# Performance work log

Measured on AMD Instinct MI355X. Metric: run time of the kernel, lower is better.

## Reference

```python
import jax, jax.numpy as jnp
import numpy as np

B, C, H, W = 32, 1024, 32, 32  # N = H*W must equal C for the attn_c * attn_s broadcast
C8 = C // 8


def setup_inputs() -> dict:
    key = jax.random.key(0)
    ks = jax.random.split(key, 9)
    s = 1.0 / np.sqrt(C)
    return {
        "z": jax.random.normal(ks[0], (B, C, H, W), jnp.float32),
        "x": jax.random.normal(ks[1], (B, C, H, W), jnp.float32),
        "y": jax.random.normal(ks[2], (B, C, H, W), jnp.float32),
        "Wq": jax.random.normal(ks[3], (C8, C), jnp.float32) * s,
        "bq": jax.random.normal(ks[4], (C8,), jnp.float32) * 0.01,
        "Wk": jax.random.normal(ks[5], (C8, C), jnp.float32) * s,
        "bk": jax.random.normal(ks[6], (C8,), jnp.float32) * 0.01,
        "Wv": jax.random.normal(ks[7], (C, C), jnp.float32) * s,
        "bv": jax.random.normal(ks[8], (C,), jnp.float32) * 0.01,
    }


def reference(z, x, y, Wq, bq, Wk, bk, Wv, bv):
    b, c, h, w = x.shape
    n = h * w
    xf = x.reshape(b, c, n)
    yf = y.reshape(b, c, n)
    zf = z.reshape(b, c, n)

    # 1x1 convs == channel matmuls
    q = jnp.einsum('oc,bcn->bon', Wq, xf) + bq[None, :, None]   # (B, C/8, N)
    k = jnp.einsum('oc,bcn->bon', Wk, yf) + bk[None, :, None]   # (B, C/8, N)

    # channel-projected spatial attention: (B, N, N)
    energy_c = jnp.einsum('bcn,bcm->bnm', q, k)
    attention_c = jax.nn.softmax(energy_c, axis=-1)

    # raw channel attention: (B, C, C)
    energy_s = jnp.einsum('bcn,bdn->bcd', xf, yf)
    energy_s = jnp.max(energy_s, axis=-1, keepdims=True) - energy_s
    attention_s = jax.nn.softmax(energy_s, axis=-1)

    # multiplicative combine + third softmax (requires N == C)
    attention = jax.nn.softmax(attention_c * attention_s, axis=-1)

    v = jnp.einsum('oc,bcn->bon', Wv, zf) + bv[None, :, None]   # (B, C, N)
    # out[b,c,m] = sum_n v[b,c,n] * attention[b,m,n]  (value @ attention^T)
    out = jnp.einsum('bcn,bmn->bcm', v, attention)
    return z + out.reshape(b, c, h, w)
```

## Files before the change

### kernel.cpp

```cpp
#include <hip/hip_runtime.h>
#include <hip/hip_bf16.h>

typedef __attribute__((ext_vector_type(8))) short s8_t;
typedef __attribute__((ext_vector_type(4))) float f4_t;

__device__ __forceinline__ unsigned short f2bf(float f) {
  union { float f; unsigned u; } x; x.f = f;
  unsigned r = x.u + 0x7fffu + ((x.u >> 16) & 1u);
  return (unsigned short)(r >> 16);
}

__device__ __forceinline__ void split2(float e0, float e1, unsigned& hp, unsigned& lp) {
  unsigned b0 = __float_as_uint(e0), b1 = __float_as_uint(e1);
  unsigned h0 = b0 & 0xFFFF0000u, h1 = b1 & 0xFFFF0000u;
  hp = (b0 >> 16) | h1;
  float l0 = e0 - __uint_as_float(h0), l1 = e1 - __uint_as_float(h1);
  lp = (__float_as_uint(l0) >> 16) | (__float_as_uint(l1) & 0xFFFF0000u);
}

__device__ __forceinline__ void gload16(const void* g, void* l) {
  __builtin_amdgcn_global_load_lds(
      (const __attribute__((address_space(1))) void*)g,
      (__attribute__((address_space(3))) void*)l, 16, 0, 0);
}

__global__ __launch_bounds__(256) void k_convert(const float* __restrict__ in,
                                                 unsigned short* __restrict__ out, int n) {
  int i = (blockIdx.x * 256 + threadIdx.x) * 8;
  if (i >= n) return;
  float4 a = *(const float4*)(in + i);
  float4 b = *(const float4*)(in + i + 4);
  ushort4 u0; u0.x = f2bf(a.x); u0.y = f2bf(a.y); u0.z = f2bf(a.z); u0.w = f2bf(a.w);
  ushort4 u1; u1.x = f2bf(b.x); u1.y = f2bf(b.y); u1.z = f2bf(b.z); u1.w = f2bf(b.w);
  *(ushort4*)(out + i) = u0;
  *(ushort4*)(out + i + 4) = u1;
}

__global__ __launch_bounds__(256) void k_transp32(const float* __restrict__ in,
                                                  float* __restrict__ out) {
  __shared__ float tile[64][65];
  const int t = threadIdx.x, b = blockIdx.z;
  const int r0 = blockIdx.y * 64, c0 = blockIdx.x * 64;
  const float* ip = in + (size_t)b * 1048576;
  float* op = out + (size_t)b * 1048576;
  const int tr = t >> 4, tc = (t & 15) * 4;
#pragma unroll
  for (int p = 0; p < 4; ++p) {
    int r = p * 16 + tr;
    float4 v = *(const float4*)(ip + (size_t)(r0 + r) * 1024 + c0 + tc);
    tile[r][tc] = v.x; tile[r][tc + 1] = v.y; tile[r][tc + 2] = v.z; tile[r][tc + 3] = v.w;
  }
  __syncthreads();
#pragma unroll
  for (int p = 0; p < 4; ++p) {
    int n = p * 16 + tr;
    float4 w;
    w.x = tile[tc][n]; w.y = tile[tc + 1][n]; w.z = tile[tc + 2][n]; w.w = tile[tc + 3][n];
    *(float4*)(op + (size_t)(c0 + n) * 1024 + r0 + tc) = w;
  }
}

__global__ __launch_bounds__(256) void k_transpbf(const float* __restrict__ in,
                                                  unsigned short* __restrict__ outt) {
  __shared__ unsigned short tile[64][72];
  const int t = threadIdx.x, b = blockIdx.z;
  const int r0 = blockIdx.y * 64, c0 = blockIdx.x * 64;
  const float* ip = in + (size_t)b * 1048576;
  const int tr = t >> 4, tc = (t & 15) * 4;
#pragma unroll
  for (int p = 0; p < 4; ++p) {
    int r = p * 16 + tr;
    float4 v = *(const float4*)(ip + (size_t)(r0 + r) * 1024 + c0 + tc);
    tile[r][tc] = f2bf(v.x); tile[r][tc + 1] = f2bf(v.y);
    tile[r][tc + 2] = f2bf(v.z); tile[r][tc + 3] = f2bf(v.w);
  }
  __syncthreads();
#pragma unroll
  for (int p = 0; p < 4; ++p) {
    int n = p * 16 + tr;
    ushort4 w;
    w.x = tile[tc][n]; w.y = tile[tc + 1][n]; w.z = tile[tc + 2][n]; w.w = tile[tc + 3][n];
    *(ushort4*)(outt + (size_t)b * 1048576 + (size_t)(c0 + n) * 1024 + r0 + tc) = w;
  }
}

template <int BIAS_MODE>
__global__ __launch_bounds__(256) void k_mfma3(
    const float* __restrict__ A, int lda, long long sA,
    const float* __restrict__ B, int ldb, long long sB,
    float* __restrict__ C, int ldc, long long sC,
    const float* __restrict__ bias, int K) {
  __shared__ __align__(16) unsigned short Ah[4096], Al[4096], Bh[4096], Bl[4096];
  const int tid = threadIdx.x;
  const int lane = tid & 63, wave = tid >> 6;
  const int wr = wave >> 1, wc = wave & 1;
  const int bz = blockIdx.z;
  const int m0 = blockIdx.x * 128, n0 = blockIdx.y * 128;

  const int sr = tid >> 1, sh = (tid & 1) * 16;
  const float* ag = A + (long long)bz * sA + (long long)(m0 + sr) * lda + sh;
  const float* bg = B + (long long)bz * sB + (long long)(n0 + sr) * ldb + sh;
  unsigned short* wah = &Ah[sr * 32 + sh];
  unsigned short* wal = &Al[sr * 32 + sh];
  unsigned short* wbh = &Bh[sr * 32 + sh];
  unsigned short* wbl = &Bl[sr * 32 + sh];

  const int lr = lane & 15, lg = lane >> 4;
  const int fa = (wr * 64 + lr) * 32 + lg * 8;
  const int fb = (wc * 64 + lr) * 32 + lg * 8;

  f4_t acc[4][4];
#pragma unroll
  for (int i = 0; i < 4; ++i)
#pragma unroll
    for (int j = 0; j < 4; ++j) acc[i][j] = (f4_t)0.f;

  for (int k0 = 0; k0 < K; k0 += 32) {
    float av[16], bv[16];
#pragma unroll
    for (int p = 0; p < 4; ++p) {
      *(float4*)(av + p * 4) = *(const float4*)(ag + p * 4);
      *(float4*)(bv + p * 4) = *(const float4*)(bg + p * 4);
    }
    unsigned ah[8], al[8], bh[8], bl[8];
#pragma unroll
    for (int p = 0; p < 8; ++p) {
      split2(av[2 * p], av[2 * p + 1], ah[p], al[p]);
      split2(bv[2 * p], bv[2 * p + 1], bh[p], bl[p]);
    }
    *(uint4*)(wah) = *(uint4*)(ah);     *(uint4*)(wah + 8) = *(uint4*)(ah + 4);
    *(uint4*)(wal) = *(uint4*)(al);     *(uint4*)(wal + 8) = *(uint4*)(al + 4);
    *(uint4*)(wbh) = *(uint4*)(bh);     *(uint4*)(wbh + 8) = *(uint4*)(bh + 4);
    *(uint4*)(wbl) = *(uint4*)(bl);     *(uint4*)(wbl + 8) = *(uint4*)(bl + 4);
    ag += 32; bg += 32;
    __syncthreads();

    s8_t fah[4], fbh[4], ftmp[4];
#pragma unroll
    for (int f = 0; f < 4; ++f) {
      fah[f] = *(const s8_t*)(Ah + fa + f * 512);
      fbh[f] = *(const s8_t*)(Bh + fb + f * 512);
    }
#pragma unroll
    for (int i = 0; i < 4; ++i)
#pragma unroll
      for (int j = 0; j < 4; ++j)
        acc[i][j] = __builtin_amdgcn_mfma_f32_16x16x32_bf16(fah[i], fbh[j], acc[i][j], 0, 0, 0);
#pragma unroll
    for (int f = 0; f < 4; ++f) ftmp[f] = *(const s8_t*)(Bl + fb + f * 512);
#pragma unroll
    for (int i = 0; i < 4; ++i)
#pragma unroll
      for (int j = 0; j < 4; ++j)
        acc[i][j] = __builtin_amdgcn_mfma_f32_16x16x32_bf16(fah[i], ftmp[j], acc[i][j], 0, 0, 0);
#pragma unroll
    for (int f = 0; f < 4; ++f) ftmp[f] = *(const s8_t*)(Al + fa + f * 512);
#pragma unroll
    for (int i = 0; i < 4; ++i)
#pragma unroll
      for (int j = 0; j < 4; ++j)
        acc[i][j] = __builtin_amdgcn_mfma_f32_16x16x32_bf16(ftmp[i], fbh[j], acc[i][j], 0, 0, 0);
    __syncthreads();
  }

#pragma unroll
  for (int i = 0; i < 4; ++i) {
    const int rbase = m0 + wr * 64 + i * 16 + lg * 4;
#pragma unroll
    for (int j = 0; j < 4; ++j) {
      const int col = n0 + wc * 64 + j * 16 + lr;
      float bc = (BIAS_MODE == 2) ? bias[col] : 0.f;
#pragma unroll
      for (int e = 0; e < 4; ++e) {
        float v = acc[i][j][e];
        if (BIAS_MODE == 2) v += bc;
        C[(long long)bz * sC + (long long)(rbase + e) * ldc + col] = v;
      }
    }
  }
}

template <int BIAS_MODE, bool OUT_BF16, bool RESID>
__global__ __launch_bounds__(256) void k_mfma(
    const unsigned short* __restrict__ A, int lda, long long sA,
    const unsigned short* __restrict__ B, int ldb, long long sB,
    void* __restrict__ Cp, int ldc, long long sC,
    const float* __restrict__ bias,
    const float* __restrict__ resid, long long sR, int K) {
  __shared__ __align__(16) unsigned short As[4096];
  __shared__ __align__(16) unsigned short Bs[4096];
  const int tid = threadIdx.x;
  const int lane = tid & 63, wave = tid >> 6;
  const int wr = wave >> 1, wc = wave & 1;
  const int bz = blockIdx.z;
  const int m0 = blockIdx.x * 128, n0 = blockIdx.y * 128;

  const int ch0 = wave * 64 + lane, ch1 = ch0 + 256;
  const unsigned short* pa0 = A + (long long)bz * sA + (long long)(m0 + (ch0 >> 2)) * lda + (ch0 & 3) * 8;
  const unsigned short* pa1 = A + (long long)bz * sA + (long long)(m0 + (ch1 >> 2)) * lda + (ch1 & 3) * 8;
  const unsigned short* pb0 = B + (long long)bz * sB + (long long)(n0 + (ch0 >> 2)) * ldb + (ch0 & 3) * 8;
  const unsigned short* pb1 = B + (long long)bz * sB + (long long)(n0 + (ch1 >> 2)) * ldb + (ch1 & 3) * 8;
  char* la0 = (char*)As + wave * 1024;
  char* la1 = la0 + 4096;
  char* lb0 = (char*)Bs + wave * 1024;
  char* lb1 = lb0 + 4096;

  const int lr = lane & 15, lg = lane >> 4;
  const unsigned short* arp = As + (wr * 64 + lr) * 32 + lg * 8;
  const unsigned short* brp = Bs + (wc * 64 + lr) * 32 + lg * 8;

  f4_t acc[4][4];
#pragma unroll
  for (int i = 0; i < 4; ++i)
#pragma unroll
    for (int j = 0; j < 4; ++j) acc[i][j] = (f4_t)0.f;

  for (int k0 = 0; k0 < K; k0 += 32) {
    gload16(pa0, la0); gload16(pa1, la1);
    gload16(pb0, lb0); gload16(pb1, lb1);
    pa0 += 32; pa1 += 32; pb0 += 32; pb1 += 32;
    __syncthreads();
    s8_t af[4], bf[4];
#pragma unroll
    for (int f = 0; f < 4; ++f) {
      af[f] = *(const s8_t*)(arp + f * 16 * 32);
      bf[f] = *(const s8_t*)(brp + f * 16 * 32);
    }
#pragma unroll
    for (int i = 0; i < 4; ++i)
#pragma unroll
      for (int j = 0; j < 4; ++j)
        acc[i][j] = __builtin_amdgcn_mfma_f32_16x16x32_bf16(af[i], bf[j], acc[i][j], 0, 0, 0);
    __syncthreads();
  }

#pragma unroll
  for (int i = 0; i < 4; ++i) {
    const int rbase = m0 + wr * 64 + i * 16 + lg * 4;
#pragma unroll
    for (int j = 0; j < 4; ++j) {
      const int col = n0 + wc * 64 + j * 16 + lr;
#pragma unroll
      for (int e = 0; e < 4; ++e) {
        const int row = rbase + e;
        float v = acc[i][j][e];
        if (BIAS_MODE == 1) v += bias[row];
        const long long off = (long long)bz * sC + (long long)row * ldc + col;
        if (RESID) v += resid[(long long)bz * sR + (long long)row * ldc + col];
        if (OUT_BF16) ((unsigned short*)Cp)[off] = f2bf(v);
        else          ((float*)Cp)[off] = v;
      }
    }
  }
}

__device__ __forceinline__ float wave_red_max(float v) {
#pragma unroll
  for (int o = 32; o > 0; o >>= 1) v = fmaxf(v, __shfl_down(v, o, 64));
  return v;
}
__device__ __forceinline__ float wave_red_sum(float v) {
#pragma unroll
  for (int o = 32; o > 0; o >>= 1) v += __shfl_down(v, o, 64);
  return v;
}
__device__ __forceinline__ float block_red_max(float v, float* red) {
  v = wave_red_max(v);
  if ((threadIdx.x & 63) == 0) red[threadIdx.x >> 6] = v;
  __syncthreads();
  v = fmaxf(fmaxf(red[0], red[1]), fmaxf(red[2], red[3]));
  __syncthreads();
  return v;
}
__device__ __forceinline__ float block_red_sum(float v, float* red) {
  v = wave_red_sum(v);
  if ((threadIdx.x & 63) == 0) red[threadIdx.x >> 6] = v;
  __syncthreads();
  v = red[0] + red[1] + red[2] + red[3];
  __syncthreads();
  return v;
}

__global__ __launch_bounds__(256) void k_combine(float* __restrict__ ec,
                                                 const float* __restrict__ es) {
  __shared__ float red[4];
  const size_t row = blockIdx.x;
  float* cp = ec + row * 1024;
  const float* sp = es + row * 1024;
  const int tid = threadIdx.x;
  float4 c4 = ((const float4*)cp)[tid];
  float4 s4 = ((const float4*)sp)[tid];

  float mx = fmaxf(fmaxf(c4.x, c4.y), fmaxf(c4.z, c4.w));
  mx = block_red_max(mx, red);
  float e0 = __expf(c4.x - mx), e1 = __expf(c4.y - mx);
  float e2 = __expf(c4.z - mx), e3 = __expf(c4.w - mx);
  float sc = block_red_sum(e0 + e1 + e2 + e3, red);

  float t0 = -s4.x, t1 = -s4.y, t2 = -s4.z, t3 = -s4.w;
  float mt = fmaxf(fmaxf(t0, t1), fmaxf(t2, t3));
  mt = block_red_max(mt, red);
  float f0 = __expf(t0 - mt), f1 = __expf(t1 - mt);
  float f2 = __expf(t2 - mt), f3 = __expf(t3 - mt);
  float ss = block_red_sum(f0 + f1 + f2 + f3, red);

  const float rc = 1.f / sc, rs = 1.f / ss;
  float g0 = __expf((e0 * rc) * (f0 * rs));
  float g1 = __expf((e1 * rc) * (f1 * rs));
  float g2 = __expf((e2 * rc) * (f2 * rs));
  float g3 = __expf((e3 * rc) * (f3 * rs));
  float s3 = block_red_sum(g0 + g1 + g2 + g3, red);
  const float r3 = 1.f / s3;
  ushort4 o;
  o.x = f2bf(g0 * r3); o.y = f2bf(g1 * r3); o.z = f2bf(g2 * r3); o.w = f2bf(g3 * r3);
  ((ushort4*)cp)[tid] = o;
}

extern "C" void kernel_launch(void* const* d_in, const int* in_sizes, int n_in,
                              void* d_out, int out_size, void* d_ws, size_t ws_size,
                              hipStream_t stream) {
  const float* z = (const float*)d_in[0];
  const float* x = (const float*)d_in[1];
  const float* y = (const float*)d_in[2];
  const float* Wq = (const float*)d_in[3];
  const float* bq = (const float*)d_in[4];
  const float* Wk = (const float*)d_in[5];
  const float* bk = (const float*)d_in[6];
  const float* Wv = (const float*)d_in[7];
  const float* bv = (const float*)d_in[8];
  float* out = (float*)d_out;

  char* ws = (char*)d_ws;
  float* es = (float*)ws;
  unsigned short* z_t = (unsigned short*)ws;
  unsigned short* v_bf = z_t + 33554432;
  char* wsB = ws + 134217728;
  float* xytf = (float*)wsB;
  float* ec = (float*)wsB;
  unsigned short* attn = (unsigned short*)wsB;
  char* wsC = ws + 268435456;
  float* q_t = (float*)wsC;
  float* k_t = q_t + 4194304;
  unsigned short* wv = (unsigned short*)wsC;

  dim3 blk(256);
  hipLaunchKernelGGL(k_transp32, dim3(16, 16, 32), blk, 0, stream, x, xytf);
  hipLaunchKernelGGL((k_mfma3<2>), dim3(8, 1, 32), blk, 0, stream,
                     xytf, 1024, 1048576LL, Wq, 1024, 0LL, q_t, 128, 131072LL, bq, 1024);
  hipLaunchKernelGGL(k_transp32, dim3(16, 16, 32), blk, 0, stream, y, xytf);
  hipLaunchKernelGGL((k_mfma3<2>), dim3(8, 1, 32), blk, 0, stream,
                     xytf, 1024, 1048576LL, Wk, 1024, 0LL, k_t, 128, 131072LL, bk, 1024);
  hipLaunchKernelGGL((k_mfma3<0>), dim3(8, 8, 32), blk, 0, stream,
                     x, 1024, 1048576LL, y, 1024, 1048576LL, es, 1024, 1048576LL,
                     (const float*)nullptr, 1024);
  hipLaunchKernelGGL((k_mfma3<0>), dim3(8, 8, 32), blk, 0, stream,
                     q_t, 128, 131072LL, k_t, 128, 131072LL, ec, 1024, 1048576LL,
                     (const float*)nullptr, 128);
  hipLaunchKernelGGL(k_combine, dim3(32768), blk, 0, stream, ec, es);
  hipLaunchKernelGGL(k_transpbf, dim3(16, 16, 32), blk, 0, stream, z, z_t);
  hipLaunchKernelGGL(k_convert, dim3(512), blk, 0, stream, Wv, wv, 1048576);
  hipLaunchKernelGGL((k_mfma<1, true, false>), dim3(8, 8, 32), blk, 0, stream,
                     wv, 1024, 0LL, z_t, 1024, 1048576LL, (void*)v_bf, 1024, 1048576LL,
                     bv, (const float*)nullptr, 0LL, 1024);
  hipLaunchKernelGGL((k_mfma<0, false, true>), dim3(8, 8, 32), blk, 0, stream,
                     v_bf, 1024, 1048576LL, attn, 2048, 2097152LL, (void*)out, 1024, 1048576LL,
                     (const float*)nullptr, z, 1048576LL, 1024);
}
```

Before: 885.7 us.

## Double-buffer LDS tiles in split-bf16 MFMA GEMM to overlap global loads

Converts the 3-pass split-bf16 MFMA GEMM main loop into a software pipeline with two LDS buffers. The next K-tile's global loads are issued before the current tile's MFMAs, and the hi/lo split plus LDS write happen after them. This hides global memory latency and removes one barrier per iteration. In exchange, LDS per block doubles to 64KB, which may reduce occupancy, and register pressure rises from holding the prefetched values.

```diff
diff --git a/kernel.cpp b/kernel.cpp
--- a/kernel.cpp
+++ b/kernel.cpp
@@ -84,13 +84,31 @@
   }
 }
 
+__device__ __forceinline__ void split_write(unsigned short* buf, int wbase,
+                                            const float* av, const float* bv) {
+  unsigned ah[8], al[8], bh[8], bl[8];
+#pragma unroll
+  for (int p = 0; p < 8; ++p) {
+    split2(av[2 * p], av[2 * p + 1], ah[p], al[p]);
+    split2(bv[2 * p], bv[2 * p + 1], bh[p], bl[p]);
+  }
+  *(uint4*)(buf + wbase) = *(uint4*)(ah);
+  *(uint4*)(buf + wbase + 8) = *(uint4*)(ah + 4);
+  *(uint4*)(buf + 4096 + wbase) = *(uint4*)(al);
+  *(uint4*)(buf + 4096 + wbase + 8) = *(uint4*)(al + 4);
+  *(uint4*)(buf + 8192 + wbase) = *(uint4*)(bh);
+  *(uint4*)(buf + 8192 + wbase + 8) = *(uint4*)(bh + 4);
+  *(uint4*)(buf + 12288 + wbase) = *(uint4*)(bl);
+  *(uint4*)(buf + 12288 + wbase + 8) = *(uint4*)(bl + 4);
+}
+
 template <int BIAS_MODE>
 __global__ __launch_bounds__(256) void k_mfma3(
     const float* __restrict__ A, int lda, long long sA,
     const float* __restrict__ B, int ldb, long long sB,
     float* __restrict__ C, int ldc, long long sC,
     const float* __restrict__ bias, int K) {
-  __shared__ __align__(16) unsigned short Ah[4096], Al[4096], Bh[4096], Bl[4096];
+  __shared__ __align__(16) unsigned short sm[32768];
   const int tid = threadIdx.x;
   const int lane = tid & 63, wave = tid >> 6;
   const int wr = wave >> 1, wc = wave & 1;
@@ -100,10 +118,7 @@
   const int sr = tid >> 1, sh = (tid & 1) * 16;
   const float* ag = A + (long long)bz * sA + (long long)(m0 + sr) * lda + sh;
   const float* bg = B + (long long)bz * sB + (long long)(n0 + sr) * ldb + sh;
-  unsigned short* wah = &Ah[sr * 32 + sh];
-  unsigned short* wal = &Al[sr * 32 + sh];
-  unsigned short* wbh = &Bh[sr * 32 + sh];
-  unsigned short* wbl = &Bl[sr * 32 + sh];
+  const int wbase = sr * 32 + sh;
 
   const int lr = lane & 15, lg = lane >> 4;
   const int fa = (wr * 64 + lr) * 32 + lg * 8;
@@ -115,31 +130,39 @@
 #pragma unroll
     for (int j = 0; j < 4; ++j) acc[i][j] = (f4_t)0.f;
 
-  for (int k0 = 0; k0 < K; k0 += 32) {
-    float av[16], bv[16];
-#pragma unroll
-    for (int p = 0; p < 4; ++p) {
-      *(float4*)(av + p * 4) = *(const float4*)(ag + p * 4);
-      *(float4*)(bv + p * 4) = *(const float4*)(bg + p * 4);
-    }
-    unsigned ah[8], al[8], bh[8], bl[8];
-#pragma unroll
-    for (int p = 0; p < 8; ++p) {
-      split2(av[2 * p], av[2 * p + 1], ah[p], al[p]);
-      split2(bv[2 * p], bv[2 * p + 1], bh[p], bl[p]);
-    }
-    *(uint4*)(wah) = *(uint4*)(ah);     *(uint4*)(wah + 8) = *(uint4*)(ah + 4);
-    *(uint4*)(wal) = *(uint4*)(al);     *(uint4*)(wal + 8) = *(uint4*)(al + 4);
-    *(uint4*)(wbh) = *(uint4*)(bh);     *(uint4*)(wbh + 8) = *(uint4*)(bh + 4);
-    *(uint4*)(wbl) = *(uint4*)(bl);     *(uint4*)(wbl + 8) = *(uint4*)(bl + 4);
-    ag += 32; bg += 32;
-    __syncthreads();
-
+  const int nt = K >> 5;
+  float av[16], bv[16];
+
+#pragma unroll
+  for (int p = 0; p < 4; ++p) {
+    *(float4*)(av + p * 4) = *(const float4*)(ag + p * 4);
+    *(float4*)(bv + p * 4) = *(const float4*)(bg + p * 4);
+  }
+  ag += 32; bg += 32;
+  split_write(sm, wbase, av, bv);
+  __syncthreads();
+
+  for (int t = 0; t < nt; ++t) {
+    unsigned short* bufc = sm + (t & 1) * 16384;
+    unsigned short* bufn = sm + ((t + 1) & 1) * 16384;
+    const bool more = (t + 1 < nt);
+    if (more) {
+#pragma unroll
+      for (int p = 0; p < 4; ++p) {
+        *(float4*)(av + p * 4) = *(const float4*)(ag + p * 4);
+        *(float4*)(bv + p * 4) = *(const float4*)(bg + p * 4);
+      }
+      ag += 32; bg += 32;
+    }
+    const unsigned short* Ahp = bufc;
+    const unsigned short* Alp = bufc + 4096;
+    const unsigned short* Bhp = bufc + 8192;
+    const unsigned short* Blp = bufc + 12288;
     s8_t fah[4], fbh[4], ftmp[4];
 #pragma unroll
     for (int f = 0; f < 4; ++f) {
-      fah[f] = *(const s8_t*)(Ah + fa + f * 512);
-      fbh[f] = *(const s8_t*)(Bh + fb + f * 512);
+      fah[f] = *(const s8_t*)(Ahp + fa + f * 512);
+      fbh[f] = *(const s8_t*)(Bhp + fb + f * 512);
     }
 #pragma unroll
     for (int i = 0; i < 4; ++i)
@@ -147,19 +170,20 @@
       for (int j = 0; j < 4; ++j)
         acc[i][j] = __builtin_amdgcn_mfma_f32_16x16x32_bf16(fah[i], fbh[j], acc[i][j], 0, 0, 0);
 #pragma unroll
-    for (int f = 0; f < 4; ++f) ftmp[f] = *(const s8_t*)(Bl + fb + f * 512);
+    for (int f = 0; f < 4; ++f) ftmp[f] = *(const s8_t*)(Blp + fb + f * 512);
 #pragma unroll
     for (int i = 0; i < 4; ++i)
 #pragma unroll
       for (int j = 0; j < 4; ++j)
         acc[i][j] = __builtin_amdgcn_mfma_f32_16x16x32_bf16(fah[i], ftmp[j], acc[i][j], 0, 0, 0);
 #pragma unroll
-    for (int f = 0; f < 4; ++f) ftmp[f] = *(const s8_t*)(Al + fa + f * 512);
+    for (int f = 0; f < 4; ++f) ftmp[f] = *(const s8_t*)(Alp + fa + f * 512);
 #pragma unroll
     for (int i = 0; i < 4; ++i)
 #pragma unroll
       for (int j = 0; j < 4; ++j)
         acc[i][j] = __builtin_amdgcn_mfma_f32_16x16x32_bf16(ftmp[i], fbh[j], acc[i][j], 0, 0, 0);
+    if (more) split_write(bufn, wbase, av, bv);
     __syncthreads();
   }
 
```

Result: slower. 953.9 us (+7.7%).

## Pre-split fp32 inputs to bf16 hi/lo planes and stream via LDS loads

Applied to the files above, without the earlier changes.

Adds a transpose-and-split kernel that writes x and y as bf16 high/low planes in both layouts. The 3-pass bf16 GEMMs then load the planes straight into LDS with global_load_lds instead of converting fp32 in registers each K-step. Q and K projections are fused into one launch that emits split outputs, and batches run in chunks of 8 so the split buffers fit the workspace. A swizzled block-index mapping is added to the GEMMs for better cache locality. In exchange it writes and rereads more intermediate data and issues more small launches.

```diff
diff --git a/kernel.cpp b/kernel.cpp
--- a/kernel.cpp
+++ b/kernel.cpp
@@ -8,6 +8,14 @@
   union { float f; unsigned u; } x; x.f = f;
   unsigned r = x.u + 0x7fffu + ((x.u >> 16) & 1u);
   return (unsigned short)(r >> 16);
+}
+
+__device__ __forceinline__ void split1(float v, unsigned short& h, unsigned short& l) {
+  unsigned b = __float_as_uint(v);
+  unsigned hb = b & 0xFFFF0000u;
+  h = (unsigned short)(b >> 16);
+  float lo = v - __uint_as_float(hb);
+  l = (unsigned short)(__float_as_uint(lo) >> 16);
 }
 
 __device__ __forceinline__ void split2(float e0, float e1, unsigned& hp, unsigned& lp) {
@@ -22,6 +30,17 @@
   __builtin_amdgcn_global_load_lds(
       (const __attribute__((address_space(1))) void*)g,
       (__attribute__((address_space(3))) void*)l, 16, 0, 0);
+}
+
+__device__ __forceinline__ void swz_grid(int& bx, int& by, int& bz) {
+  const int gx = gridDim.x, gy = gridDim.y;
+  const int nwg = gx * gy * gridDim.z;
+  const int flat = (blockIdx.z * gy + blockIdx.y) * gx + blockIdx.x;
+  const int s = (flat & 7) * (nwg >> 3) + (flat >> 3);
+  bx = s % gx;
+  const int r = s / gx;
+  by = r % gy;
+  bz = r / gy;
 }
 
 __global__ __launch_bounds__(256) void k_convert(const float* __restrict__ in,
@@ -36,27 +55,37 @@
   *(ushort4*)(out + i + 4) = u1;
 }
 
-__global__ __launch_bounds__(256) void k_transp32(const float* __restrict__ in,
-                                                  float* __restrict__ out) {
+__global__ __launch_bounds__(256) void k_tsplit(const float* __restrict__ in,
+                                                unsigned short* __restrict__ nh,
+                                                unsigned short* __restrict__ nl,
+                                                unsigned short* __restrict__ th,
+                                                unsigned short* __restrict__ tl) {
   __shared__ float tile[64][65];
-  const int t = threadIdx.x, b = blockIdx.z;
+  const int t = threadIdx.x, bz = blockIdx.z;
   const int r0 = blockIdx.y * 64, c0 = blockIdx.x * 64;
-  const float* ip = in + (size_t)b * 1048576;
-  float* op = out + (size_t)b * 1048576;
+  const float* ip = in + (size_t)bz * 1048576;
+  const size_t ob = (size_t)bz * 1048576;
   const int tr = t >> 4, tc = (t & 15) * 4;
 #pragma unroll
   for (int p = 0; p < 4; ++p) {
     int r = p * 16 + tr;
     float4 v = *(const float4*)(ip + (size_t)(r0 + r) * 1024 + c0 + tc);
+    ushort4 h, l;
+    split1(v.x, h.x, l.x); split1(v.y, h.y, l.y);
+    split1(v.z, h.z, l.z); split1(v.w, h.w, l.w);
+    *(ushort4*)(nh + ob + (size_t)(r0 + r) * 1024 + c0 + tc) = h;
+    *(ushort4*)(nl + ob + (size_t)(r0 + r) * 1024 + c0 + tc) = l;
     tile[r][tc] = v.x; tile[r][tc + 1] = v.y; tile[r][tc + 2] = v.z; tile[r][tc + 3] = v.w;
   }
   __syncthreads();
 #pragma unroll
   for (int p = 0; p < 4; ++p) {
     int n = p * 16 + tr;
-    float4 w;
-    w.x = tile[tc][n]; w.y = tile[tc + 1][n]; w.z = tile[tc + 2][n]; w.w = tile[tc + 3][n];
-    *(float4*)(op + (size_t)(c0 + n) * 1024 + r0 + tc) = w;
+    float a = tile[tc][n], b = tile[tc + 1][n], c = tile[tc + 2][n], d = tile[tc + 3][n];
+    ushort4 h, l;
+    split1(a, h.x, l.x); split1(b, h.y, l.y); split1(c, h.z, l.z); split1(d, h.w, l.w);
+    *(ushort4*)(th + ob + (size_t)(c0 + n) * 1024 + r0 + tc) = h;
+    *(ushort4*)(tl + ob + (size_t)(c0 + n) * 1024 + r0 + tc) = l;
   }
 }
 
@@ -84,26 +113,32 @@
   }
 }
 
-template <int BIAS_MODE>
-__global__ __launch_bounds__(256) void k_mfma3(
-    const float* __restrict__ A, int lda, long long sA,
-    const float* __restrict__ B, int ldb, long long sB,
-    float* __restrict__ C, int ldc, long long sC,
-    const float* __restrict__ bias, int K) {
-  __shared__ __align__(16) unsigned short Ah[4096], Al[4096], Bh[4096], Bl[4096];
-  const int tid = threadIdx.x;
-  const int lane = tid & 63, wave = tid >> 6;
+__global__ __launch_bounds__(256) void k_es3p(
+    const unsigned short* __restrict__ Ah, const unsigned short* __restrict__ Al,
+    long long sA, int lda,
+    const unsigned short* __restrict__ Bh, const unsigned short* __restrict__ Bl,
+    long long sB, int ldb,
+    float* __restrict__ C, int ldc, long long sC, int K) {
+  __shared__ __align__(16) unsigned short smAh[4096], smAl[4096], smBh[4096], smBl[4096];
+  int bx, by, bz; swz_grid(bx, by, bz);
+  const int tid = threadIdx.x, lane = tid & 63, wave = tid >> 6;
   const int wr = wave >> 1, wc = wave & 1;
-  const int bz = blockIdx.z;
-  const int m0 = blockIdx.x * 128, n0 = blockIdx.y * 128;
-
-  const int sr = tid >> 1, sh = (tid & 1) * 16;
-  const float* ag = A + (long long)bz * sA + (long long)(m0 + sr) * lda + sh;
-  const float* bg = B + (long long)bz * sB + (long long)(n0 + sr) * ldb + sh;
-  unsigned short* wah = &Ah[sr * 32 + sh];
-  unsigned short* wal = &Al[sr * 32 + sh];
-  unsigned short* wbh = &Bh[sr * 32 + sh];
-  unsigned short* wbl = &Bl[sr * 32 + sh];
+  const int m0 = bx * 128, n0 = by * 128;
+
+  const int ch0 = wave * 64 + lane, ch1 = ch0 + 256;
+  const int r0 = ch0 >> 2, kc0 = (ch0 & 3) * 8, r1 = ch1 >> 2, kc1 = (ch1 & 3) * 8;
+  const unsigned short* pah0 = Ah + (long long)bz * sA + (long long)(m0 + r0) * lda + kc0;
+  const unsigned short* pah1 = Ah + (long long)bz * sA + (long long)(m0 + r1) * lda + kc1;
+  const unsigned short* pal0 = Al + (long long)bz * sA + (long long)(m0 + r0) * lda + kc0;
+  const unsigned short* pal1 = Al + (long long)bz * sA + (long long)(m0 + r1) * lda + kc1;
+  const unsigned short* pbh0 = Bh + (long long)bz * sB + (long long)(n0 + r0) * ldb + kc0;
+  const unsigned short* pbh1 = Bh + (long long)bz * sB + (long long)(n0 + r1) * ldb + kc1;
+  const unsigned short* pbl0 = Bl + (long long)bz * sB + (long long)(n0 + r0) * ldb + kc0;
+  const unsigned short* pbl1 = Bl + (long long)bz * sB + (long long)(n0 + r1) * ldb + kc1;
+  char* dAh0 = (char*)smAh + wave * 1024; char* dAh1 = dAh0 + 4096;
+  char* dAl0 = (char*)smAl + wave * 1024; char* dAl1 = dAl0 + 4096;
+  char* dBh0 = (char*)smBh + wave * 1024; char* dBh1 = dBh0 + 4096;
+  char* dBl0 = (char*)smBl + wave * 1024; char* dBl1 = dBl0 + 4096;
 
   const int lr = lane & 15, lg = lane >> 4;
   const int fa = (wr * 64 + lr) * 32 + lg * 8;
@@ -116,50 +151,38 @@
     for (int j = 0; j < 4; ++j) acc[i][j] = (f4_t)0.f;
 
   for (int k0 = 0; k0 < K; k0 += 32) {
-    float av[16], bv[16];
-#pragma unroll
-    for (int p = 0; p < 4; ++p) {
-      *(float4*)(av + p * 4) = *(const float4*)(ag + p * 4);
-      *(float4*)(bv + p * 4) = *(const float4*)(bg + p * 4);
+    gload16(pah0, dAh0); gload16(pah1, dAh1);
+    gload16(pal0, dAl0); gload16(pal1, dAl1);
+    gload16(pbh0, dBh0); gload16(pbh1, dBh1);
+    gload16(pbl0, dBl0); gload16(pbl1, dBl1);
+    pah0 += 32; pah1 += 32; pal0 += 32; pal1 += 32;
+    pbh0 += 32; pbh1 += 32; pbl0 += 32; pbl1 += 32;
+    __syncthreads();
+    s8_t fah[4], fbh[4], ft[4];
+#pragma unroll
+    for (int f = 0; f < 4; ++f) {
+      fah[f] = *(const s8_t*)(smAh + fa + f * 512);
+      fbh[f] = *(const s8_t*)(smBh + fb + f * 512);
     }
-    unsigned ah[8], al[8], bh[8], bl[8];
-#pragma unroll
-    for (int p = 0; p < 8; ++p) {
-      split2(av[2 * p], av[2 * p + 1], ah[p], al[p]);
-      split2(bv[2 * p], bv[2 * p + 1], bh[p], bl[p]);
-    }
-    *(uint4*)(wah) = *(uint4*)(ah);     *(uint4*)(wah + 8) = *(uint4*)(ah + 4);
-    *(uint4*)(wal) = *(uint4*)(al);     *(uint4*)(wal + 8) = *(uint4*)(al + 4);
-    *(uint4*)(wbh) = *(uint4*)(bh);     *(uint4*)(wbh + 8) = *(uint4*)(bh + 4);
-    *(uint4*)(wbl) = *(uint4*)(bl);     *(uint4*)(wbl + 8) = *(uint4*)(bl + 4);
-    ag += 32; bg += 32;
-    __syncthreads();
-
-    s8_t fah[4], fbh[4], ftmp[4];
-#pragma unroll
-    for (int f = 0; f < 4; ++f) {
-      fah[f] = *(const s8_t*)(Ah + fa + f * 512);
-      fbh[f] = *(const s8_t*)(Bh + fb + f * 512);
-    }
 #pragma unroll
     for (int i = 0; i < 4; ++i)
 #pragma unroll
       for (int j = 0; j < 4; ++j)
         acc[i][j] = __builtin_amdgcn_mfma_f32_16x16x32_bf16(fah[i], fbh[j], acc[i][j], 0, 0, 0);
 #pragma unroll
-    for (int f = 0; f < 4; ++f) ftmp[f] = *(const s8_t*)(Bl + fb + f * 512);
-#pragma unroll
-    for (int i = 0; i < 4; ++i)
-#pragma unroll
-      for (int j = 0; j < 4; ++j)
-        acc[i][j] = __builtin_amdgcn_mfma_f32_16x16x32_bf16(fah[i], ftmp[j], acc[i][j], 0, 0, 0);
-#pragma unroll
-    for (int f = 0; f < 4; ++f) ftmp[f] = *(const s8_t*)(Al + fa + f * 512);
-#pragma unroll
-    for (int i = 0; i < 4; ++i)
-#pragma unroll
-      for (int j = 0; j < 4; ++j)
-        acc[i][j] = __builtin_amdgcn_mfma_f32_16x16x32_bf16(ftmp[i], fbh[j], acc[i][j], 0, 0, 0);
+    for (int f = 0; f < 4; ++f) ft[f] = *(const s8_t*)(smBl + fb + f * 512);
+#pragma unroll
+    for (int i = 0; i < 4; ++i)
+#pragma unroll
+      for (int j = 0; j < 4; ++j)
+        acc[i][j] = __builtin_amdgcn_mfma_f32_16x16x32_bf16(fah[i], ft[j], acc[i][j], 0, 0, 0);
+#pragma unroll
+    for (int f = 0; f < 4; ++f) ft[f] = *(const s8_t*)(smAl + fa + f * 512);
+#pragma unroll
+    for (int i = 0; i < 4; ++i)
+#pragma unroll
+      for (int j = 0; j < 4; ++j)
+        acc[i][j] = __builtin_amdgcn_mfma_f32_16x16x32_bf16(ft[i], fbh[j], acc[i][j], 0, 0, 0);
     __syncthreads();
   }
 
@@ -169,12 +192,115 @@
 #pragma unroll
     for (int j = 0; j < 4; ++j) {
       const int col = n0 + wc * 64 + j * 16 + lr;
-      float bc = (BIAS_MODE == 2) ? bias[col] : 0.f;
+#pragma unroll
+      for (int e = 0; e < 4; ++e)
+        C[(long long)bz * sC + (long long)(rbase + e) * ldc + col] = acc[i][j][e];
+    }
+  }
+}
+
+__global__ __launch_bounds__(256) void k_qk3p(
+    const unsigned short* __restrict__ Axh, const unsigned short* __restrict__ Axl,
+    const unsigned short* __restrict__ Ayh, const unsigned short* __restrict__ Ayl,
+    const float* __restrict__ Wqf, const float* __restrict__ Wkf,
+    const float* __restrict__ bqf, const float* __restrict__ bkf,
+    unsigned short* __restrict__ Qh, unsigned short* __restrict__ Ql,
+    unsigned short* __restrict__ Kh, unsigned short* __restrict__ Kl) {
+  __shared__ __align__(16) unsigned short smAh[4096], smAl[4096], smBh[4096], smBl[4096];
+  int bx, by, bz; swz_grid(bx, by, bz);
+  const unsigned short* Ah = by ? Ayh : Axh;
+  const unsigned short* Al = by ? Ayl : Axl;
+  const float* Bf = by ? Wkf : Wqf;
+  const float* bias = by ? bkf : bqf;
+  unsigned short* Oh = by ? Kh : Qh;
+  unsigned short* Ol = by ? Kl : Ql;
+
+  const int tid = threadIdx.x, lane = tid & 63, wave = tid >> 6;
+  const int wr = wave >> 1, wc = wave & 1;
+  const int m0 = bx * 128;
+
+  const int ch0 = wave * 64 + lane, ch1 = ch0 + 256;
+  const int r0 = ch0 >> 2, kc0 = (ch0 & 3) * 8, r1 = ch1 >> 2, kc1 = (ch1 & 3) * 8;
+  const unsigned short* pah0 = Ah + (long long)bz * 1048576 + (long long)(m0 + r0) * 1024 + kc0;
+  const unsigned short* pah1 = Ah + (long long)bz * 1048576 + (long long)(m0 + r1) * 1024 + kc1;
+  const unsigned short* pal0 = Al + (long long)bz * 1048576 + (long long)(m0 + r0) * 1024 + kc0;
+  const unsigned short* pal1 = Al + (long long)bz * 1048576 + (long long)(m0 + r1) * 1024 + kc1;
+  char* dAh0 = (char*)smAh + wave * 1024; char* dAh1 = dAh0 + 4096;
+  char* dAl0 = (char*)smAl + wave * 1024; char* dAl1 = dAl0 + 4096;
+
+  const int sr = tid >> 1, sh = (tid & 1) * 16;
+  const float* bg = Bf + (long long)sr * 1024 + sh;
+  const int wbase = sr * 32 + sh;
+
+  const int lr = lane & 15, lg = lane >> 4;
+  const int fa = (wr * 64 + lr) * 32 + lg * 8;
+  const int fb = (wc * 64 + lr) * 32 + lg * 8;
+
+  f4_t acc[4][4];
+#pragma unroll
+  for (int i = 0; i < 4; ++i)
+#pragma unroll
+    for (int j = 0; j < 4; ++j) acc[i][j] = (f4_t)0.f;
+
+  for (int k0 = 0; k0 < 1024; k0 += 32) {
+    gload16(pah0, dAh0); gload16(pah1, dAh1);
+    gload16(pal0, dAl0); gload16(pal1, dAl1);
+    pah0 += 32; pah1 += 32; pal0 += 32; pal1 += 32;
+    float bv[16];
+#pragma unroll
+    for (int p = 0; p < 4; ++p) *(float4*)(bv + p * 4) = *(const float4*)(bg + p * 4);
+    bg += 32;
+    unsigned bh[8], bl[8];
+#pragma unroll
+    for (int p = 0; p < 8; ++p) split2(bv[2 * p], bv[2 * p + 1], bh[p], bl[p]);
+    *(uint4*)(smBh + wbase) = *(uint4*)(bh);
+    *(uint4*)(smBh + wbase + 8) = *(uint4*)(bh + 4);
+    *(uint4*)(smBl + wbase) = *(uint4*)(bl);
+    *(uint4*)(smBl + wbase + 8) = *(uint4*)(bl + 4);
+    __syncthreads();
+    s8_t fah[4], fbh[4], ft[4];
+#pragma unroll
+    for (int f = 0; f < 4; ++f) {
+      fah[f] = *(const s8_t*)(smAh + fa + f * 512);
+      fbh[f] = *(const s8_t*)(smBh + fb + f * 512);
+    }
+#pragma unroll
+    for (int i = 0; i < 4; ++i)
+#pragma unroll
+      for (int j = 0; j < 4; ++j)
+        acc[i][j] = __builtin_amdgcn_mfma_f32_16x16x32_bf16(fah[i], fbh[j], acc[i][j], 0, 0, 0);
+#pragma unroll
+    for (int f = 0; f < 4; ++f) ft[f] = *(const s8_t*)(smBl + fb + f * 512);
+#pragma unroll
+    for (int i = 0; i < 4; ++i)
+#pragma unroll
+      for (int j = 0; j < 4; ++j)
+        acc[i][j] = __builtin_amdgcn_mfma_f32_16x16x32_bf16(fah[i], ft[j], acc[i][j], 0, 0, 0);
+#pragma unroll
+    for (int f = 0; f < 4; ++f) ft[f] = *(const s8_t*)(smAl + fa + f * 512);
+#pragma unroll
+    for (int i = 0; i < 4; ++i)
+#pragma unroll
+      for (int j = 0; j < 4; ++j)
+        acc[i][j] = __builtin_amdgcn_mfma_f32_16x16x32_bf16(ft[i], fbh[j], acc[i][j], 0, 0, 0);
+    __syncthreads();
+  }
+
+#pragma unroll
+  for (int i = 0; i < 4; ++i) {
+    const int rbase = m0 + wr * 64 + i * 16 + lg * 4;
+#pragma unroll
+    for (int j = 0; j < 4; ++j) {
+      const int col = wc * 64 + j * 16 + lr;
+      const float bc = bias[col];
 #pragma unroll
       for (int e = 0; e < 4; ++e) {
-        float v = acc[i][j][e];
-        if (BIAS_MODE == 2) v += bc;
-        C[(long long)bz * sC + (long long)(rbase + e) * ldc + col] = v;
+        float v = acc[i][j][e] + bc;
+        unsigned short h, l;
+        split1(v, h, l);
+        const long long off = (long long)bz * 131072 + (long long)(rbase + e) * 128 + col;
+        Oh[off] = h;
+        Ol[off] = l;
       }
     }
   }
@@ -189,11 +315,11 @@
     const float* __restrict__ resid, long long sR, int K) {
   __shared__ __align__(16) unsigned short As[4096];
   __shared__ __align__(16) unsigned short Bs[4096];
+  int bxs, bys, bz; swz_grid(bxs, bys, bz);
   const int tid = threadIdx.x;
   const int lane = tid & 63, wave = tid >> 6;
   const int wr = wave >> 1, wc = wave & 1;
-  const int bz = blockIdx.z;
-  const int m0 = blockIdx.x * 128, n0 = blockIdx.y * 128;
+  const int m0 = bxs * 128, n0 = bys * 128;
 
   const int ch0 = wave * 64 + lane, ch1 = ch0 + 256;
   const unsigned short* pa0 = A + (long long)bz * sA + (long long)(m0 + (ch0 >> 2)) * lda + (ch0 & 3) * 8;
@@ -335,27 +461,39 @@
   unsigned short* z_t = (unsigned short*)ws;
   unsigned short* v_bf = z_t + 33554432;
   char* wsB = ws + 134217728;
-  float* xytf = (float*)wsB;
+  unsigned short* xh  = (unsigned short*)wsB;
+  unsigned short* xl  = xh + 8388608;
+  unsigned short* yh  = xl + 8388608;
+  unsigned short* yl  = yh + 8388608;
+  unsigned short* xth = yl + 8388608;
+  unsigned short* xtl = xth + 8388608;
+  unsigned short* yth = xtl + 8388608;
+  unsigned short* ytl = yth + 8388608;
   float* ec = (float*)wsB;
   unsigned short* attn = (unsigned short*)wsB;
   char* wsC = ws + 268435456;
-  float* q_t = (float*)wsC;
-  float* k_t = q_t + 4194304;
+  unsigned short* qh = (unsigned short*)wsC;
+  unsigned short* ql = qh + 4194304;
+  unsigned short* kh = ql + 4194304;
+  unsigned short* kl = kh + 4194304;
   unsigned short* wv = (unsigned short*)wsC;
 
   dim3 blk(256);
-  hipLaunchKernelGGL(k_transp32, dim3(16, 16, 32), blk, 0, stream, x, xytf);
-  hipLaunchKernelGGL((k_mfma3<2>), dim3(8, 1, 32), blk, 0, stream,
-                     xytf, 1024, 1048576LL, Wq, 1024, 0LL, q_t, 128, 131072LL, bq, 1024);
-  hipLaunchKernelGGL(k_transp32, dim3(16, 16, 32), blk, 0, stream, y, xytf);
-  hipLaunchKernelGGL((k_mfma3<2>), dim3(8, 1, 32), blk, 0, stream,
-                     xytf, 1024, 1048576LL, Wk, 1024, 0LL, k_t, 128, 131072LL, bk, 1024);
-  hipLaunchKernelGGL((k_mfma3<0>), dim3(8, 8, 32), blk, 0, stream,
-                     x, 1024, 1048576LL, y, 1024, 1048576LL, es, 1024, 1048576LL,
-                     (const float*)nullptr, 1024);
-  hipLaunchKernelGGL((k_mfma3<0>), dim3(8, 8, 32), blk, 0, stream,
-                     q_t, 128, 131072LL, k_t, 128, 131072LL, ec, 1024, 1048576LL,
-                     (const float*)nullptr, 128);
+  for (int c = 0; c < 4; ++c) {
+    const size_t boff = (size_t)c * 8 * 1048576;
+    hipLaunchKernelGGL(k_tsplit, dim3(16, 16, 8), blk, 0, stream, x + boff, xh, xl, xth, xtl);
+    hipLaunchKernelGGL(k_tsplit, dim3(16, 16, 8), blk, 0, stream, y + boff, yh, yl, yth, ytl);
+    hipLaunchKernelGGL(k_es3p, dim3(8, 8, 8), blk, 0, stream,
+                       xh, xl, 1048576LL, 1024, yh, yl, 1048576LL, 1024,
+                       es + boff, 1024, 1048576LL, 1024);
+    hipLaunchKernelGGL(k_qk3p, dim3(8, 2, 8), blk, 0, stream,
+                       xth, xtl, yth, ytl, Wq, Wk, bq, bk,
+                       qh + c * 8 * 131072, ql + c * 8 * 131072,
+                       kh + c * 8 * 131072, kl + c * 8 * 131072);
+  }
+  hipLaunchKernelGGL(k_es3p, dim3(8, 8, 32), blk, 0, stream,
+                     qh, ql, 131072LL, 128, kh, kl, 131072LL, 128,
+                     ec, 1024, 1048576LL, 128);
   hipLaunchKernelGGL(k_combine, dim3(32768), blk, 0, stream, ec, es);
   hipLaunchKernelGGL(k_transpbf, dim3(16, 16, 32), blk, 0, stream, z, z_t);
   hipLaunchKernelGGL(k_convert, dim3(512), blk, 0, stream, Wv, wv, 1048576);
```

Result: slower. 1.004 ms (+13.4%).
